# Performance work log

Hardware: AMD Instinct MI355X
Metric: run time of the kernel (lower is better)

Reference implementation:

```python
import jax, jax.numpy as jnp
import numpy as np


def setup_inputs() -> dict:
    key = jax.random.key(0)
    ks = jax.random.split(key, 8)
    B, T, U = 4, 256, 128
    De, Dp, D, V = 512, 512, 640, 1024
    s = lambda k, sh, fan: jax.random.normal(k, sh, dtype=jnp.float32) / np.sqrt(fan)
    return {
        "enc": jax.random.normal(ks[0], (B, T, De), dtype=jnp.float32),
        "pred": jax.random.normal(ks[1], (B, U, Dp), dtype=jnp.float32),
        "W_enc": s(ks[2], (De, D), De),
        "b_enc": jnp.zeros((D,), jnp.float32),
        "W_pred": s(ks[3], (Dp, D), Dp),
        "b_pred": jnp.zeros((D,), jnp.float32),
        "W_joint": s(ks[4], (D, V), D),
        "b_joint": jnp.zeros((V,), jnp.float32),
    }


def reference(enc, pred, W_enc, b_enc, W_pred, b_pred, W_joint, b_joint):
    # f: [B,T,D], g: [B,U,D]
    f = jnp.einsum("bte,ed->btd", enc, W_enc) + b_enc
    g = jnp.einsum("bup,pd->bud", pred, W_pred) + b_pred
    # broadcast-add over the T x U lattice, tanh activation
    joint = jnp.tanh(f[:, :, None, :] + g[:, None, :, :])  # [B,T,U,D]
    # final projection to num_classes
    out = jnp.einsum("btud,dv->btuv", joint, W_joint) + b_joint  # [B,T,U,V]
    return out
```

## Files before the change

kernel.cpp:

```cpp
#include <hip/hip_runtime.h>
#include <hip/hip_bf16.h>
#include <stdint.h>

typedef unsigned short u16;
typedef __attribute__((ext_vector_type(8))) __bf16 bf16x8;
typedef __attribute__((ext_vector_type(4))) float f32x4;
typedef __attribute__((ext_vector_type(16))) float f32x16;
typedef __attribute__((ext_vector_type(8))) unsigned short u16x8;
typedef __attribute__((ext_vector_type(4))) unsigned int u32x4;

static __device__ __forceinline__ u16 f2bf(float x) {
  __hip_bfloat16 h = __float2bfloat16(x);
  u16 u;
  __builtin_memcpy(&u, &h, 2);
  return u;
}

static __device__ __forceinline__ float fast_tanh(float x) {
  float e = __expf(2.0f * x);
  return 1.0f - 2.0f * __builtin_amdgcn_rcpf(e + 1.0f);
}

static __device__ __forceinline__ void gload_lds16(const void* g, void* l) {
  __builtin_amdgcn_global_load_lds(
      (const __attribute__((address_space(1))) unsigned int*)g,
      (__attribute__((address_space(3))) unsigned int*)l, 16, 0, 0);
}

static __device__ __forceinline__ int swz(int row, int byte_in_row) {
  return row * 128 + (byte_in_row ^ ((row & 7) << 4));
}

__global__ __launch_bounds__(256) void transpose_cast_kernel(
    const float* __restrict__ in, u16* __restrict__ out, int K, int N) {
  int n = blockIdx.x;
  for (int k = threadIdx.x; k < K; k += 256) {
    out[(size_t)n * K + k] = f2bf(in[(size_t)k * N + n]);
  }
}

__global__ __launch_bounds__(256) void linear_kernel(
    const float* __restrict__ A, const u16* __restrict__ Wt,
    const float* __restrict__ bias, float* __restrict__ out) {
  __shared__ u16 sA[64 * 64];
  __shared__ u16 sB[64 * 64];
  const int t = threadIdx.x;
  const int bx = blockIdx.x;
  const int m0 = (bx / 10) * 64;
  const int n0 = (bx % 10) * 64;
  const int lane = t & 63, wid = t >> 6;
  const int wr = wid >> 1, wc = wid & 1;
  const int l15 = lane & 15, lk8 = (lane >> 4) << 3;

  const int srow = t >> 2;
  const int kc = (t & 3) << 4;

  f32x4 acc[2][2] = {};

  for (int k0 = 0; k0 < 512; k0 += 64) {
    {
      const float4* gp = (const float4*)(A + (size_t)(m0 + srow) * 512 + k0 + kc);
      u16 tmp[16];
#pragma unroll
      for (int i = 0; i < 4; ++i) {
        float4 v = gp[i];
        tmp[i * 4 + 0] = f2bf(v.x);
        tmp[i * 4 + 1] = f2bf(v.y);
        tmp[i * 4 + 2] = f2bf(v.z);
        tmp[i * 4 + 3] = f2bf(v.w);
      }
      *(u16x8*)((char*)sA + swz(srow, kc * 2)) = *(u16x8*)&tmp[0];
      *(u16x8*)((char*)sA + swz(srow, kc * 2 + 16)) = *(u16x8*)&tmp[8];
    }
    {
      const int off = (t & 3) << 5;
      const char* gsrc = (const char*)Wt + ((size_t)(n0 + srow) * 512 + k0) * 2 + off;
      u32x4 q0 = *(const u32x4*)gsrc;
      u32x4 q1 = *(const u32x4*)(gsrc + 16);
      *(u32x4*)((char*)sB + swz(srow, off)) = q0;
      *(u32x4*)((char*)sB + swz(srow, off + 16)) = q1;
    }
    __syncthreads();
#pragma unroll
    for (int kh = 0; kh < 2; ++kh) {
      const int kbyte = kh * 64 + lk8 * 2;
      bf16x8 av[2], bv[2];
#pragma unroll
      for (int mf = 0; mf < 2; ++mf)
        av[mf] = *(const bf16x8*)((char*)sA + swz(wr * 32 + mf * 16 + l15, kbyte));
#pragma unroll
      for (int nf = 0; nf < 2; ++nf)
        bv[nf] = *(const bf16x8*)((char*)sB + swz(wc * 32 + nf * 16 + l15, kbyte));
#pragma unroll
      for (int mf = 0; mf < 2; ++mf)
#pragma unroll
        for (int nf = 0; nf < 2; ++nf)
          acc[mf][nf] = __builtin_amdgcn_mfma_f32_16x16x32_bf16(
              av[mf], bv[nf], acc[mf][nf], 0, 0, 0);
    }
    __syncthreads();
  }

  const int r4 = (lane >> 4) << 2;
#pragma unroll
  for (int nf = 0; nf < 2; ++nf) {
    const int nc = n0 + wc * 32 + nf * 16 + l15;
    const float bjv = bias[nc];
#pragma unroll
    for (int mf = 0; mf < 2; ++mf) {
      const int mr = m0 + wr * 32 + mf * 16 + r4;
#pragma unroll
      for (int r = 0; r < 4; ++r)
        out[(size_t)(mr + r) * 640 + nc] = acc[mf][nf][r] + bjv;
    }
  }
}

__global__ __launch_bounds__(256) void joint_kernel(
    const float* __restrict__ f, const float* __restrict__ g,
    u16* __restrict__ joint, int m_base) {
  int idx = blockIdx.x * 256 + threadIdx.x;
  int row = idx / 80;
  int kc = (idx % 80) * 8;
  int m = m_base + row;
  int bt = m >> 7;
  int b = bt >> 8;
  int u = m & 127;
  const float4* fp = (const float4*)(f + (size_t)bt * 640 + kc);
  const float4* gp = (const float4*)(g + ((size_t)(b * 128 + u)) * 640 + kc);
  u16 tmp[8];
#pragma unroll
  for (int i = 0; i < 2; ++i) {
    float4 fv = fp[i];
    float4 gv = gp[i];
    tmp[i * 4 + 0] = f2bf(fast_tanh(fv.x + gv.x));
    tmp[i * 4 + 1] = f2bf(fast_tanh(fv.y + gv.y));
    tmp[i * 4 + 2] = f2bf(fast_tanh(fv.z + gv.z));
    tmp[i * 4 + 3] = f2bf(fast_tanh(fv.w + gv.w));
  }
  *(u16x8*)(joint + (size_t)row * 640 + kc) = *(u16x8*)&tmp[0];
}

__global__ __launch_bounds__(512, 2) void gemm256_kernel(
    const u16* __restrict__ A,
    const u16* __restrict__ Bt,
    const float* __restrict__ bias,
    float* __restrict__ out,
    int m_base, int mtiles) {
  extern __shared__ char smem[];
  const int t = threadIdx.x;
  const int lane = t & 63, wid = t >> 6;

  const int nwg = mtiles * 4;
  const int bid = blockIdx.x;
  const int q = nwg >> 3, r = nwg & 7;
  const int xcd = bid & 7, local = bid >> 3;
  const int wgid = (xcd < r ? xcd * (q + 1) : r * (q + 1) + (xcd - r) * q) + local;
  const int mt = wgid >> 2, nt = wgid & 3;

  const int wr = wid >> 2, wc = wid & 3;
  const int l31 = lane & 31, hi = lane >> 5;
  const int rx = (lane & 7) << 4;

  const int srow = t >> 3;
  const int xc = ((t & 7) ^ ((t >> 3) & 7)) << 4;
  const u16* aSrc[4];
  const u16* bSrc[4];
#pragma unroll
  for (int j = 0; j < 4; ++j) {
    const int row = j * 64 + srow;
    aSrc[j] = A + (size_t)(mt * 256 + row) * 640 + (xc >> 1);
    bSrc[j] = Bt + (size_t)(nt * 256 + row) * 640 + (xc >> 1);
  }
  const int sdst = wid * 1024;

  f32x16 acc[4][2] = {};

#pragma unroll
  for (int j = 0; j < 4; ++j) {
    gload_lds16(aSrc[j], smem + j * 8192 + sdst);
    gload_lds16(bSrc[j], smem + 32768 + j * 8192 + sdst);
  }
  __syncthreads();

  for (int tt = 0; tt < 10; ++tt) {
    const int bufo = (tt & 1) * 65536;
    if (tt < 9) {
      const int ke = (tt + 1) * 64;
      const int nbufo = bufo ^ 65536;
#pragma unroll
      for (int j = 0; j < 4; ++j) {
        gload_lds16(aSrc[j] + ke, smem + nbufo + j * 8192 + sdst);
        gload_lds16(bSrc[j] + ke, smem + nbufo + 32768 + j * 8192 + sdst);
      }
    }
    const char* sA = smem + bufo;
    const char* sB = smem + bufo + 32768;
#pragma unroll
    for (int ks = 0; ks < 4; ++ks) {
      const int cb = (ks * 32 + (hi << 4)) ^ rx;
      bf16x8 bv[2], av[4];
#pragma unroll
      for (int nn = 0; nn < 2; ++nn)
        bv[nn] = *(const bf16x8*)(sB + (wc * 64 + nn * 32 + l31) * 128 + cb);
#pragma unroll
      for (int mm = 0; mm < 4; ++mm)
        av[mm] = *(const bf16x8*)(sA + (wr * 128 + mm * 32 + l31) * 128 + cb);
      __builtin_amdgcn_s_setprio(1);
#pragma unroll
      for (int mm = 0; mm < 4; ++mm)
#pragma unroll
        for (int nn = 0; nn < 2; ++nn)
          acc[mm][nn] = __builtin_amdgcn_mfma_f32_32x32x16_bf16(
              av[mm], bv[nn], acc[mm][nn], 0, 0, 0);
      __builtin_amdgcn_s_setprio(0);
    }
    if (tt < 9) __syncthreads();
  }

#pragma unroll
  for (int nn = 0; nn < 2; ++nn) {
    const int v = nt * 256 + wc * 64 + nn * 32 + l31;
    const float bjv = bias[v];
#pragma unroll
    for (int mm = 0; mm < 4; ++mm) {
      const size_t mrow =
          (size_t)m_base + (size_t)mt * 256 + wr * 128 + mm * 32 + hi * 4;
#pragma unroll
      for (int reg = 0; reg < 16; ++reg) {
        const int row = (reg & 3) + 8 * (reg >> 2);
        out[(mrow + row) * 1024 + v] = acc[mm][nn][reg] + bjv;
      }
    }
  }
}

__global__ __launch_bounds__(512) void fused_joint_kernel(
    const float* __restrict__ f, const float* __restrict__ g,
    const u16* __restrict__ Wjt, const float* __restrict__ bj,
    float* __restrict__ out) {
  __shared__ u16 sA[128 * 64];
  __shared__ u16 sB[256 * 64];
  const int t = threadIdx.x;
  const int bt = blockIdx.x;
  const int b = bt >> 8;
  const int v0 = blockIdx.y << 8;
  const float* frow = f + (size_t)bt * 640;
  const float* gbase = g + (size_t)b * 128 * 640;

  const int lane = t & 63, wid = t >> 6;
  const int wr = wid >> 2, wc = wid & 3;
  const int l15 = lane & 15, lk8 = (lane >> 4) << 3;

  const int au = t >> 2;
  const int akc = (t & 3) << 4;
  const int bn = t >> 1;
  const int boff = (t & 1) << 6;

  f32x4 acc[4][4] = {};

  for (int k0 = 0; k0 < 640; k0 += 64) {
    {
      const float4* gp = (const float4*)(gbase + (size_t)au * 640 + k0 + akc);
      const float4* fp = (const float4*)(frow + k0 + akc);
      u16 tmp[16];
#pragma unroll
      for (int i = 0; i < 4; ++i) {
        float4 gv = gp[i];
        float4 fv = fp[i];
        tmp[i * 4 + 0] = f2bf(fast_tanh(gv.x + fv.x));
        tmp[i * 4 + 1] = f2bf(fast_tanh(gv.y + fv.y));
        tmp[i * 4 + 2] = f2bf(fast_tanh(gv.z + fv.z));
        tmp[i * 4 + 3] = f2bf(fast_tanh(gv.w + fv.w));
      }
      *(u16x8*)((char*)sA + swz(au, akc * 2)) = *(u16x8*)&tmp[0];
      *(u16x8*)((char*)sA + swz(au, akc * 2 + 16)) = *(u16x8*)&tmp[8];
    }
    {
      const char* gsrc = (const char*)Wjt + ((size_t)(v0 + bn) * 640 + k0) * 2 + boff;
#pragma unroll
      for (int i = 0; i < 4; ++i) {
        u32x4 qv = *(const u32x4*)(gsrc + i * 16);
        *(u32x4*)((char*)sB + swz(bn, boff + i * 16)) = qv;
      }
    }
    __syncthreads();
#pragma unroll
    for (int kh = 0; kh < 2; ++kh) {
      const int kbyte = kh * 64 + lk8 * 2;
      bf16x8 av[4], bv[4];
#pragma unroll
      for (int mf = 0; mf < 4; ++mf)
        av[mf] = *(const bf16x8*)((char*)sA + swz(wr * 64 + mf * 16 + l15, kbyte));
#pragma unroll
      for (int nf = 0; nf < 4; ++nf)
        bv[nf] = *(const bf16x8*)((char*)sB + swz(wc * 64 + nf * 16 + l15, kbyte));
#pragma unroll
      for (int mf = 0; mf < 4; ++mf)
#pragma unroll
        for (int nf = 0; nf < 4; ++nf)
          acc[mf][nf] = __builtin_amdgcn_mfma_f32_16x16x32_bf16(
              av[mf], bv[nf], acc[mf][nf], 0, 0, 0);
    }
    __syncthreads();
  }

  const int r4 = (lane >> 4) << 2;
#pragma unroll
  for (int nf = 0; nf < 4; ++nf) {
    const int v = v0 + wc * 64 + nf * 16 + l15;
    const float bjv = bj[v];
#pragma unroll
    for (int mf = 0; mf < 4; ++mf) {
      const int u = wr * 64 + mf * 16 + r4;
      const size_t o = ((size_t)bt * 128 + u) * 1024 + v;
#pragma unroll
      for (int rr = 0; rr < 4; ++rr)
        out[o + (size_t)rr * 1024] = acc[mf][nf][rr] + bjv;
    }
  }
}

extern "C" void kernel_launch(void* const* d_in, const int* in_sizes, int n_in,
                              void* d_out, int out_size, void* d_ws, size_t ws_size,
                              hipStream_t stream) {
  const float* enc = (const float*)d_in[0];
  const float* pred = (const float*)d_in[1];
  const float* W_enc = (const float*)d_in[2];
  const float* b_enc = (const float*)d_in[3];
  const float* W_pred = (const float*)d_in[4];
  const float* b_pred = (const float*)d_in[5];
  const float* W_joint = (const float*)d_in[6];
  const float* b_joint = (const float*)d_in[7];
  float* out = (float*)d_out;

  char* ws = (char*)d_ws;
  float* f = (float*)ws;
  float* gbuf = (float*)(ws + 2621440);
  u16* Wet = (u16*)(ws + 2621440 + 1310720);
  u16* Wpt = (u16*)(ws + 2621440 + 1310720 + 655360);
  u16* Wjt = (u16*)(ws + 2621440 + 1310720 + 2 * 655360);
  const size_t fixed = 2621440 + 1310720 + 2 * 655360 + 1310720;
  u16* joint = (u16*)(ws + fixed);

  transpose_cast_kernel<<<640, 256, 0, stream>>>(W_enc, Wet, 512, 640);
  transpose_cast_kernel<<<640, 256, 0, stream>>>(W_pred, Wpt, 512, 640);
  transpose_cast_kernel<<<1024, 256, 0, stream>>>(W_joint, Wjt, 640, 1024);

  linear_kernel<<<16 * 10, 256, 0, stream>>>(enc, Wet, b_enc, f);
  linear_kernel<<<8 * 10, 256, 0, stream>>>(pred, Wpt, b_pred, gbuf);

  const long TOTAL_M = 131072;
  long maxrows = ws_size > fixed ? (long)((ws_size - fixed) / 1280) : 0;
  maxrows &= ~255L;

  if (maxrows >= 16384) {
    (void)hipFuncSetAttribute((const void*)gemm256_kernel,
                              hipFuncAttributeMaxDynamicSharedMemorySize, 131072);
    long CH = maxrows < 32768 ? maxrows : 32768;
    for (long m0 = 0; m0 < TOTAL_M; m0 += CH) {
      long R = TOTAL_M - m0 < CH ? TOTAL_M - m0 : CH;
      int mtiles = (int)(R / 256);
      joint_kernel<<<(int)(R / 128) * 40, 256, 0, stream>>>(f, gbuf, joint, (int)m0);
      gemm256_kernel<<<mtiles * 4, 512, 131072, stream>>>(joint, Wjt, b_joint, out,
                                                          (int)m0, mtiles);
    }
  } else {
    fused_joint_kernel<<<dim3(1024, 4), 512, 0, stream>>>(f, gbuf, Wjt, b_joint, out);
  }
}
```

Baseline: 335.2 us.

## Load B operand directly from global into registers, halve GEMM LDS

```diff
diff --git a/kernel.cpp b/kernel.cpp
--- a/kernel.cpp
+++ b/kernel.cpp
@@ -165,44 +165,45 @@
   const int srow = t >> 3;
   const int xc = ((t & 7) ^ ((t >> 3) & 7)) << 4;
   const u16* aSrc[4];
-  const u16* bSrc[4];
-#pragma unroll
-  for (int j = 0; j < 4; ++j) {
-    const int row = j * 64 + srow;
-    aSrc[j] = A + (size_t)(mt * 256 + row) * 640 + (xc >> 1);
-    bSrc[j] = Bt + (size_t)(nt * 256 + row) * 640 + (xc >> 1);
-  }
+#pragma unroll
+  for (int j = 0; j < 4; ++j)
+    aSrc[j] = A + (size_t)(mt * 256 + j * 64 + srow) * 640 + (xc >> 1);
   const int sdst = wid * 1024;
 
+  const u16* bG = Bt + (size_t)(nt * 256 + wc * 64 + l31) * 640 + (hi << 3);
+
   f32x16 acc[4][2] = {};
-
-#pragma unroll
-  for (int j = 0; j < 4; ++j) {
-    gload_lds16(aSrc[j], smem + j * 8192 + sdst);
-    gload_lds16(bSrc[j], smem + 32768 + j * 8192 + sdst);
-  }
+  bf16x8 bReg[2][2][4];
+
+#pragma unroll
+  for (int j = 0; j < 4; ++j) gload_lds16(aSrc[j], smem + j * 8192 + sdst);
+#pragma unroll
+  for (int nn = 0; nn < 2; ++nn)
+#pragma unroll
+    for (int ks = 0; ks < 4; ++ks)
+      bReg[0][nn][ks] = *(const bf16x8*)(bG + nn * 20480 + ks * 16);
   __syncthreads();
 
+#pragma unroll
   for (int tt = 0; tt < 10; ++tt) {
-    const int bufo = (tt & 1) * 65536;
+    const int cur = tt & 1, nxt = cur ^ 1;
     if (tt < 9) {
       const int ke = (tt + 1) * 64;
-      const int nbufo = bufo ^ 65536;
-#pragma unroll
-      for (int j = 0; j < 4; ++j) {
-        gload_lds16(aSrc[j] + ke, smem + nbufo + j * 8192 + sdst);
-        gload_lds16(bSrc[j] + ke, smem + nbufo + 32768 + j * 8192 + sdst);
-      }
-    }
-    const char* sA = smem + bufo;
-    const char* sB = smem + bufo + 32768;
+#pragma unroll
+      for (int j = 0; j < 4; ++j)
+        gload_lds16(aSrc[j] + ke, smem + nxt * 32768 + j * 8192 + sdst);
+#pragma unroll
+      for (int nn = 0; nn < 2; ++nn)
+#pragma unroll
+        for (int ks = 0; ks < 4; ++ks)
+          bReg[nxt][nn][ks] =
+              *(const bf16x8*)(bG + nn * 20480 + ke + ks * 16);
+    }
+    const char* sA = smem + cur * 32768;
 #pragma unroll
     for (int ks = 0; ks < 4; ++ks) {
       const int cb = (ks * 32 + (hi << 4)) ^ rx;
-      bf16x8 bv[2], av[4];
-#pragma unroll
-      for (int nn = 0; nn < 2; ++nn)
-        bv[nn] = *(const bf16x8*)(sB + (wc * 64 + nn * 32 + l31) * 128 + cb);
+      bf16x8 av[4];
 #pragma unroll
       for (int mm = 0; mm < 4; ++mm)
         av[mm] = *(const bf16x8*)(sA + (wr * 128 + mm * 32 + l31) * 128 + cb);
@@ -212,7 +213,7 @@
 #pragma unroll
         for (int nn = 0; nn < 2; ++nn)
           acc[mm][nn] = __builtin_amdgcn_mfma_f32_32x32x16_bf16(
-              av[mm], bv[nn], acc[mm][nn], 0, 0, 0);
+              av[mm], bReg[cur][nn][ks], acc[mm][nn], 0, 0, 0);
       __builtin_amdgcn_s_setprio(0);
     }
     if (tt < 9) __syncthreads();
@@ -356,14 +357,14 @@
 
   if (maxrows >= 16384) {
     (void)hipFuncSetAttribute((const void*)gemm256_kernel,
-                              hipFuncAttributeMaxDynamicSharedMemorySize, 131072);
+                              hipFuncAttributeMaxDynamicSharedMemorySize, 65536);
     long CH = maxrows < 32768 ? maxrows : 32768;
     for (long m0 = 0; m0 < TOTAL_M; m0 += CH) {
       long R = TOTAL_M - m0 < CH ? TOTAL_M - m0 : CH;
       int mtiles = (int)(R / 256);
       joint_kernel<<<(int)(R / 128) * 40, 256, 0, stream>>>(f, gbuf, joint, (int)m0);
-      gemm256_kernel<<<mtiles * 4, 512, 131072, stream>>>(joint, Wjt, b_joint, out,
-                                                          (int)m0, mtiles);
+      gemm256_kernel<<<mtiles * 4, 512, 65536, stream>>>(joint, Wjt, b_joint, out,
+                                                         (int)m0, mtiles);
     }
   } else {
     fused_joint_kernel<<<dim3(1024, 4), 512, 0, stream>>>(f, gbuf, Wjt, b_joint, out);
```

New measurement: 392.0 us. 1.17x slower.
